# Performance work log

Hardware: AMD Instinct MI355X
Metric: run time of the kernel (lower is better)

## Reference

```python
import jax, jax.numpy as jnp
import numpy as np

NUM_EMBEDDINGS = 1024
EMBEDDING_DIM = 512
SAMPLE_TOKENS = 4
CODE_DIM = EMBEDDING_DIM // SAMPLE_TOKENS  # 128
COMMITMENT_COST = 0.25


def setup_inputs() -> dict:
    key = jax.random.key(0)
    k1, k2 = jax.random.split(key)
    inputs = jax.random.normal(k1, (16, 1024, EMBEDDING_DIM), dtype=jnp.float32)
    # nn.Embedding weight init: uniform(-1/K, 1/K)
    emb_weight = jax.random.uniform(
        k2, (NUM_EMBEDDINGS, CODE_DIM), dtype=jnp.float32,
        minval=-1.0 / NUM_EMBEDDINGS, maxval=1.0 / NUM_EMBEDDINGS)
    return {"inputs": inputs, "emb_weight": emb_weight}


def reference(inputs, emb_weight):
    input_shape = inputs.shape
    flat = inputs.reshape(-1, CODE_DIM)  # [N, d]
    distances = (jnp.sum(flat * flat, axis=1, keepdims=True)
                 + jnp.sum(emb_weight * emb_weight, axis=1)
                 - 2.0 * jnp.matmul(flat, emb_weight.T))  # [N, K]
    encoding_indices = jnp.argmin(distances, axis=1)  # [N]
    # gather codebook rows instead of one-hot matmul (same math)
    quantized = jnp.take(emb_weight, encoding_indices, axis=0).reshape(input_shape)

    e_latent_loss = jnp.mean((jax.lax.stop_gradient(quantized) - inputs) ** 2)
    q_latent_loss = jnp.mean((quantized - jax.lax.stop_gradient(inputs)) ** 2)
    loss = q_latent_loss + COMMITMENT_COST * e_latent_loss

    # straight-through estimator
    quantized_ste = inputs + jax.lax.stop_gradient(quantized - inputs)

    # avg_probs = mean of one-hot encodings = code-usage histogram / N
    n = flat.shape[0]
    counts = jnp.zeros((NUM_EMBEDDINGS,), dtype=jnp.float32).at[encoding_indices].add(1.0)
    avg_probs = counts / n
    perplexity = jnp.exp(-jnp.sum(avg_probs * jnp.log(avg_probs + 1e-10)))

    return (quantized_ste, loss, perplexity)
```

## Files before the change

### kernel.cpp

```cpp
#include <hip/hip_runtime.h>
#include <cmath>

#define DIM      128
#define NELEMS   8388608
#define BAND_INT 12288

typedef __attribute__((ext_vector_type(8))) short  short8;
typedef __attribute__((ext_vector_type(4))) float  f32x4;


__device__ inline unsigned short f2bf(float x) {
    unsigned u = __float_as_uint(x);
    unsigned r = u + 0x7FFFu + ((u >> 16) & 1u);
    return (unsigned short)(r >> 16);
}

__global__ __launch_bounds__(256) void vq_prep_kernel(
        const float* __restrict__ e, unsigned short* __restrict__ Ehi,
        float* __restrict__ Bsq, int* __restrict__ counts, double* __restrict__ sse) {
    const int tid = threadIdx.x;
    {
        const int t  = blockIdx.x * 256 + tid;
        const int c  = t >> 4;
        const int gs = t & 15;
        const int kt = gs >> 2, qd = gs & 3;
        const int d0 = gs * 8;
        const float4 v0 = *(const float4*)(e + c * DIM + d0);
        const float4 v1 = *(const float4*)(e + c * DIM + d0 + 4);
        float f[8] = {v0.x, v0.y, v0.z, v0.w, v1.x, v1.y, v1.z, v1.w};
        unsigned short h[8];
        #pragma unroll
        for (int j = 0; j < 8; ++j) h[j] = f2bf(f[j]);
        const int ct = c >> 4, n = c & 15;
        uint4 ph;
        ph.x = h[0] | (h[1] << 16); ph.y = h[2] | (h[3] << 16);
        ph.z = h[4] | (h[5] << 16); ph.w = h[6] | (h[7] << 16);
        *(uint4*)&Ehi[(((ct * 4 + kt) * 64 + qd * 16 + n) * 8)] = ph;
    }
    {
        const int lane = tid & 31;
        #pragma unroll
        for (int r2 = 0; r2 < 2; ++r2) {
            const int row = blockIdx.x * 16 + (tid >> 5) * 2 + r2;
            const float4 xv = *(const float4*)(e + (size_t)row * DIM + lane * 4);
            float s = xv.x * xv.x + xv.y * xv.y + xv.z * xv.z + xv.w * xv.w;
            #pragma unroll
            for (int off = 16; off > 0; off >>= 1) s += __shfl_xor(s, off);
            if (lane == 0) Bsq[row] = s;
        }
    }
    if (blockIdx.x == 0) {
        ((int4*)counts)[tid] = make_int4(0, 0, 0, 0);
        if (tid == 0) *sse = 0.0;
    }
}

#define LOADPAIR(BUF, P)                                                        \
    do {                                                                        \
        const unsigned short* _bp = Ehi + (size_t)(P) * 4096;                   \
        _Pragma("unroll")                                                       \
        for (int _c = 0; _c < 2; ++_c)                                          \
            _Pragma("unroll")                                                   \
            for (int _kt = 0; _kt < 4; ++_kt)                                   \
                BUF[_c][_kt] = *(const short8*)&_bp[((_c * 4 + _kt) * 64 + lane) * 8]; \
    } while (0)

#define COMPUTEPAIR(BUF, P)                                                     \
    do {                                                                        \
        _Pragma("unroll")                                                       \
        for (int _c = 0; _c < 2; ++_c) {                                        \
            const int _ct = 2 * (P) + _c;                                       \
            f32x4 _a0 = cinit, _a1 = cinit;                                     \
            _Pragma("unroll")                                                   \
            for (int _kt = 0; _kt < 4; ++_kt) {                                 \
                _a0 = __builtin_amdgcn_mfma_f32_16x16x32_bf16(Af[0][_kt], BUF[_c][_kt], _a0, 0, 0, 0); \
                _a1 = __builtin_amdgcn_mfma_f32_16x16x32_bf16(Af[1][_kt], BUF[_c][_kt], _a1, 0, 0, 0); \
            }                                                                   \
            _Pragma("unroll")                                                   \
            for (int _r = 0; _r < 4; ++_r) {                                    \
                const int _k0 = (__float_as_int(_a0[_r]) & (int)0xFFFFFFC0) | _ct; \
                const int _t0 = min(K1[_r], _k0);                               \
                K1[_r] = max(K1[_r], _k0);                                      \
                K2[_r] = max(K2[_r], _t0);                                      \
                const int _k1 = (__float_as_int(_a1[_r]) & (int)0xFFFFFFC0) | _ct; \
                const int _t1 = min(K1[4 + _r], _k1);                           \
                K1[4 + _r] = max(K1[4 + _r], _k1);                              \
                K2[4 + _r] = max(K2[4 + _r], _t1);                              \
            }                                                                   \
        }                                                                       \
    } while (0)

__global__ __launch_bounds__(256) void vq_main_kernel(
        const float* __restrict__ x, const float* __restrict__ emb,
        const unsigned short* __restrict__ Ehi, const float* __restrict__ Bsq,
        int* __restrict__ counts, double* __restrict__ sse,
        float* __restrict__ out) {
    __shared__ __align__(16) unsigned short Xs[8448];
    __shared__ float sAsq[64];
    __shared__ int   sidx[64];

    const int tid  = threadIdx.x;
    const int wave = tid >> 6;
    const int lane = tid & 63;
    const int n    = lane & 15;
    const int quad = lane >> 4;
    const int row0 = blockIdx.x * 64;

    {
        const int rl = tid >> 3, tq = tid & 7;
        const int dbase = tq * 16;
        const int rg_lo = rl >> 4, m = rl & 15;
        #pragma unroll
        for (int w = 0; w < 2; ++w) {
            const int r = 32 * w + rl;
            const float* xp = x + (size_t)(row0 + r) * DIM + dbase;
            float p[4];
            #pragma unroll
            for (int q = 0; q < 4; ++q) {
                const float4 v = *(const float4*)(xp + 4 * q);
                p[q] = v.x * v.x + v.y * v.y + v.z * v.z + v.w * v.w;
                const int dd = dbase + 4 * q;
                const int kt = dd >> 5, qd = (dd >> 3) & 3, j = dd & 7;
                unsigned short h0 = f2bf(v.x), h1 = f2bf(v.y), h2 = f2bf(v.z), h3 = f2bf(v.w);
                uint2 ph;
                ph.x = h0 | (h1 << 16); ph.y = h2 | (h3 << 16);
                const int rg = w * 2 + rg_lo;
                *(uint2*)&Xs[(((rg * 4 + kt) * 64 + qd * 16 + m) * 8) + j] = ph;
            }
            #pragma unroll
            for (int q = 0; q < 4; ++q) p[q] += __shfl_xor(p[q], 4);
            #pragma unroll
            for (int q = 0; q < 4; ++q) p[q] += __shfl_xor(p[q], 2);
            #pragma unroll
            for (int q = 0; q < 4; ++q) p[q] += __shfl_xor(p[q], 1);
            const float s = (p[0] + p[2]) + (p[1] + p[3]);
            if (tq == 0) sAsq[r] = s;
        }
    }
    __syncthreads();

    short8 Af[2][4];
    {
        const int h = wave & 1;
        #pragma unroll
        for (int rti = 0; rti < 2; ++rti)
            #pragma unroll
            for (int kt = 0; kt < 4; ++kt)
                Af[rti][kt] = *(const short8*)&Xs[((((h * 2 + rti) * 4 + kt) * 64 + lane) * 8)];
    }
    __syncthreads();

    int K1[8], K2[8];
    #pragma unroll
    for (int i = 0; i < 8; ++i) { K1[i] = (int)0x80000000; K2[i] = (int)0x80000000; }

    const f32x4 cinit = {1.0f, 1.0f, 1.0f, 1.0f};

    short8 BfA[2][4], BfB[2][4];
    const int pbase = (wave >> 1) * 16;
    LOADPAIR(BfA, pbase);
    for (int u = 0; u < 8; ++u) {
        const int pA = pbase + 2 * u, pB = pA + 1;
        LOADPAIR(BfB, pB);
        COMPUTEPAIR(BfA, pA);
        if (u < 7) LOADPAIR(BfA, pA + 2);
        COMPUTEPAIR(BfB, pB);
    }

    int2* sc = (int2*)Xs;
    #pragma unroll
    for (int r8 = 0; r8 < 8; ++r8) {
        const int lr = 32 * (wave & 1) + 16 * (r8 >> 2) + quad * 4 + (r8 & 3);
        sc[lr * 33 + (wave >> 1) * 16 + n] = make_int2(K1[r8], K2[r8]);
    }
    __syncthreads();

    if (tid < 64) {
        const int row  = tid;
        const int rowg = row0 + row;
        const int2* ent = (const int2*)sc + row * 33;
        int mx = (int)0x80000000;
        #pragma unroll
        for (int e2 = 0; e2 < 32; ++e2) mx = max(mx, ent[e2].x);
        const int thr = mx - BAND_INT;
        int ck[8];
        int nc = 0;
        #pragma unroll
        for (int e2 = 0; e2 < 32; ++e2) {
            const int2 kk = ent[e2];
            const int ne = e2 & 15;
            if (kk.x >= thr && nc < 8) ck[nc++] = ((kk.x & 63) << 4) | ne;
            if (kk.y >= thr && nc < 8) ck[nc++] = ((kk.y & 63) << 4) | ne;
        }
        float bd = INFINITY;
        int   bk = 0x7fffffff;
        const float4* xr = (const float4*)(x + (size_t)rowg * DIM);
        const float   aq = sAsq[row];
        for (int c = 0; c < nc; ++c) {
            const int k = ck[c];
            const float4* er = (const float4*)(emb + (size_t)k * DIM);
            float acc = 0.0f;
            #pragma unroll 4
            for (int dd = 0; dd < 32; ++dd) {
                const float4 xv = xr[dd];
                const float4 ev = er[dd];
                acc += xv.x * ev.x;
                acc += xv.y * ev.y;
                acc += xv.z * ev.z;
                acc += xv.w * ev.w;
            }
            const float t    = aq + Bsq[k];
            const float dist = t - 2.0f * acc;
            if (dist < bd || (dist == bd && k < bk)) { bd = dist; bk = k; }
        }
        sidx[row] = bk;
        atomicAdd(&counts[bk], 1);
        float ss = bd;
        #pragma unroll
        for (int off = 32; off > 0; off >>= 1) ss += __shfl_down(ss, off);
        if (tid == 0) atomicAdd(sse, (double)ss);
    }
    __syncthreads();

    #pragma unroll
    for (int i = tid; i < 2048; i += 256) {
        const int row = i >> 5, d4 = i & 31;
        const int k = sidx[row];
        const float4 xv = *((const float4*)(x + (size_t)(row0 + row) * DIM) + d4);
        const float4 qv = *((const float4*)emb + (size_t)k * 32 + d4);
        float4 ov;
        ov.x = xv.x + (qv.x - xv.x);
        ov.y = xv.y + (qv.y - xv.y);
        ov.z = xv.z + (qv.z - xv.z);
        ov.w = xv.w + (qv.w - xv.w);
        *((float4*)out + (size_t)(row0 + row) * 32 + d4) = ov;
    }
}

__global__ __launch_bounds__(1024) void vq_finalize_kernel(
        const int* __restrict__ counts, const double* __restrict__ sse,
        float* __restrict__ out_tail) {
    __shared__ double red[1024];
    const int t = threadIdx.x;
    const float p = (float)counts[t] * (1.0f / 65536.0f);
    red[t] = (double)p * log((double)p + 1e-10);
    __syncthreads();
    for (int s = 512; s > 0; s >>= 1) {
        if (t < s) red[t] += red[t + s];
        __syncthreads();
    }
    if (t == 0) {
        const float m = (float)(*sse * (1.0 / 8388608.0));
        out_tail[0] = m + 0.25f * m;
        out_tail[1] = (float)exp(-red[0]);
    }
}

extern "C" void kernel_launch(void* const* d_in, const int* in_sizes, int n_in,
                              void* d_out, int out_size, void* d_ws, size_t ws_size,
                              hipStream_t stream) {
    const float* x   = (const float*)d_in[0];
    const float* emb = (const float*)d_in[1];
    float* out = (float*)d_out;

    char*           ws     = (char*)d_ws;
    float*          Bsq    = (float*)(ws + 0);
    int*            counts = (int*)(ws + 4096);
    double*         sse    = (double*)(ws + 8192);
    unsigned short* Ehi    = (unsigned short*)(ws + 16384);

    vq_prep_kernel<<<64, 256, 0, stream>>>(emb, Ehi, Bsq, counts, sse);
    vq_main_kernel<<<1024, 256, 0, stream>>>(x, emb, Ehi, Bsq, counts, sse, out);
    vq_finalize_kernel<<<1, 1024, 0, stream>>>(counts, sse, out + NELEMS);
}
```

Before: 155.5 us.

## Fold finalize into main kernel via last-block counter; single-tile B pipeline

Removes the separate finalize launch: each main-kernel block bumps an atomic done counter, and the last block computes the perplexity and loss reductions. The codebook B-fragment pipeline also changes from double-buffered pairs of column tiles to single tiles, which halves the registers held for B. This trades one kernel launch and its dependency gap for a threadfence plus an atomic in every block, and adds a serial tail run by one block.

```diff
diff --git a/kernel.cpp b/kernel.cpp
--- a/kernel.cpp
+++ b/kernel.cpp
@@ -4,6 +4,7 @@
 #define DIM      128
 #define NELEMS   8388608
 #define BAND_INT 12288
+#define NBLOCKS  1024
 
 typedef __attribute__((ext_vector_type(8))) short  short8;
 typedef __attribute__((ext_vector_type(4))) float  f32x4;
@@ -17,7 +18,8 @@
 
 __global__ __launch_bounds__(256) void vq_prep_kernel(
         const float* __restrict__ e, unsigned short* __restrict__ Ehi,
-        float* __restrict__ Bsq, int* __restrict__ counts, double* __restrict__ sse) {
+        float* __restrict__ Bsq, int* __restrict__ counts, double* __restrict__ sse,
+        int* __restrict__ done) {
     const int tid = threadIdx.x;
     {
         const int t  = blockIdx.x * 256 + tid;
@@ -51,42 +53,37 @@
     }
     if (blockIdx.x == 0) {
         ((int4*)counts)[tid] = make_int4(0, 0, 0, 0);
-        if (tid == 0) *sse = 0.0;
-    }
-}
-
-#define LOADPAIR(BUF, P)                                                        \
+        if (tid == 0) { *sse = 0.0; *done = 0; }
+    }
+}
+
+#define LOADCT(BUF, C)                                                          \
     do {                                                                        \
-        const unsigned short* _bp = Ehi + (size_t)(P) * 4096;                   \
+        const unsigned short* _bp = Ehi + (size_t)(C) * 2048;                   \
         _Pragma("unroll")                                                       \
-        for (int _c = 0; _c < 2; ++_c)                                          \
-            _Pragma("unroll")                                                   \
-            for (int _kt = 0; _kt < 4; ++_kt)                                   \
-                BUF[_c][_kt] = *(const short8*)&_bp[((_c * 4 + _kt) * 64 + lane) * 8]; \
+        for (int _kt = 0; _kt < 4; ++_kt)                                       \
+            BUF[_kt] = *(const short8*)&_bp[(_kt * 64 + lane) * 8];             \
     } while (0)
 
-#define COMPUTEPAIR(BUF, P)                                                     \
+#define COMPUTECT(BUF, C)                                                       \
     do {                                                                        \
+        const int _ct = (C);                                                    \
+        f32x4 _a0 = cinit, _a1 = cinit;                                         \
         _Pragma("unroll")                                                       \
-        for (int _c = 0; _c < 2; ++_c) {                                        \
-            const int _ct = 2 * (P) + _c;                                       \
-            f32x4 _a0 = cinit, _a1 = cinit;                                     \
-            _Pragma("unroll")                                                   \
-            for (int _kt = 0; _kt < 4; ++_kt) {                                 \
-                _a0 = __builtin_amdgcn_mfma_f32_16x16x32_bf16(Af[0][_kt], BUF[_c][_kt], _a0, 0, 0, 0); \
-                _a1 = __builtin_amdgcn_mfma_f32_16x16x32_bf16(Af[1][_kt], BUF[_c][_kt], _a1, 0, 0, 0); \
-            }                                                                   \
-            _Pragma("unroll")                                                   \
-            for (int _r = 0; _r < 4; ++_r) {                                    \
-                const int _k0 = (__float_as_int(_a0[_r]) & (int)0xFFFFFFC0) | _ct; \
-                const int _t0 = min(K1[_r], _k0);                               \
-                K1[_r] = max(K1[_r], _k0);                                      \
-                K2[_r] = max(K2[_r], _t0);                                      \
-                const int _k1 = (__float_as_int(_a1[_r]) & (int)0xFFFFFFC0) | _ct; \
-                const int _t1 = min(K1[4 + _r], _k1);                           \
-                K1[4 + _r] = max(K1[4 + _r], _k1);                              \
-                K2[4 + _r] = max(K2[4 + _r], _t1);                              \
-            }                                                                   \
+        for (int _kt = 0; _kt < 4; ++_kt) {                                     \
+            _a0 = __builtin_amdgcn_mfma_f32_16x16x32_bf16(Af[0][_kt], BUF[_kt], _a0, 0, 0, 0); \
+            _a1 = __builtin_amdgcn_mfma_f32_16x16x32_bf16(Af[1][_kt], BUF[_kt], _a1, 0, 0, 0); \
+        }                                                                       \
+        _Pragma("unroll")                                                       \
+        for (int _r = 0; _r < 4; ++_r) {                                        \
+            const int _k0 = (__float_as_int(_a0[_r]) & (int)0xFFFFFFC0) | _ct;  \
+            const int _t0 = min(K1[_r], _k0);                                   \
+            K1[_r] = max(K1[_r], _k0);                                          \
+            K2[_r] = max(K2[_r], _t0);                                          \
+            const int _k1 = (__float_as_int(_a1[_r]) & (int)0xFFFFFFC0) | _ct;  \
+            const int _t1 = min(K1[4 + _r], _k1);                               \
+            K1[4 + _r] = max(K1[4 + _r], _k1);                                  \
+            K2[4 + _r] = max(K2[4 + _r], _t1);                                  \
         }                                                                       \
     } while (0)
 
@@ -94,10 +91,12 @@
         const float* __restrict__ x, const float* __restrict__ emb,
         const unsigned short* __restrict__ Ehi, const float* __restrict__ Bsq,
         int* __restrict__ counts, double* __restrict__ sse,
-        float* __restrict__ out) {
+        int* __restrict__ done, float* __restrict__ out) {
     __shared__ __align__(16) unsigned short Xs[8448];
-    __shared__ float sAsq[64];
-    __shared__ int   sidx[64];
+    __shared__ float  sAsq[64];
+    __shared__ int    sidx[64];
+    __shared__ int    sIsLast;
+    __shared__ double red[256];
 
     const int tid  = threadIdx.x;
     const int wave = tid >> 6;
@@ -156,15 +155,15 @@
 
     const f32x4 cinit = {1.0f, 1.0f, 1.0f, 1.0f};
 
-    short8 BfA[2][4], BfB[2][4];
-    const int pbase = (wave >> 1) * 16;
-    LOADPAIR(BfA, pbase);
-    for (int u = 0; u < 8; ++u) {
-        const int pA = pbase + 2 * u, pB = pA + 1;
-        LOADPAIR(BfB, pB);
-        COMPUTEPAIR(BfA, pA);
-        if (u < 7) LOADPAIR(BfA, pA + 2);
-        COMPUTEPAIR(BfB, pB);
+    short8 BfX[4], BfY[4];
+    const int c0 = (wave >> 1) * 32;
+    LOADCT(BfX, c0);
+    for (int u = 0; u < 16; ++u) {
+        const int cA = c0 + 2 * u, cB = cA + 1;
+        LOADCT(BfY, cB);
+        COMPUTECT(BfX, cA);
+        if (u < 15) LOADCT(BfX, cA + 2);
+        COMPUTECT(BfY, cB);
     }
 
     int2* sc = (int2*)Xs;
@@ -235,24 +234,29 @@
         ov.w = xv.w + (qv.w - xv.w);
         *((float4*)out + (size_t)(row0 + row) * 32 + d4) = ov;
     }
-}
-
-__global__ __launch_bounds__(1024) void vq_finalize_kernel(
-        const int* __restrict__ counts, const double* __restrict__ sse,
-        float* __restrict__ out_tail) {
-    __shared__ double red[1024];
-    const int t = threadIdx.x;
-    const float p = (float)counts[t] * (1.0f / 65536.0f);
-    red[t] = (double)p * log((double)p + 1e-10);
-    __syncthreads();
-    for (int s = 512; s > 0; s >>= 1) {
-        if (t < s) red[t] += red[t + s];
+
+    __threadfence();
+    if (tid == 0) sIsLast = (atomicAdd(done, 1) == NBLOCKS - 1);
+    __syncthreads();
+    if (sIsLast) {
+        __threadfence();
+        double s = 0.0;
+        #pragma unroll
+        for (int k = tid; k < 1024; k += 256) {
+            const float p = (float)counts[k] * (1.0f / 65536.0f);
+            s += (double)p * log((double)p + 1e-10);
+        }
+        red[tid] = s;
         __syncthreads();
-    }
-    if (t == 0) {
-        const float m = (float)(*sse * (1.0 / 8388608.0));
-        out_tail[0] = m + 0.25f * m;
-        out_tail[1] = (float)exp(-red[0]);
+        for (int st = 128; st > 0; st >>= 1) {
+            if (tid < st) red[tid] += red[tid + st];
+            __syncthreads();
+        }
+        if (tid == 0) {
+            const float m = (float)(*sse * (1.0 / 8388608.0));
+            out[NELEMS]     = m + 0.25f * m;
+            out[NELEMS + 1] = (float)exp(-red[0]);
+        }
     }
 }
 
@@ -267,9 +271,9 @@
     float*          Bsq    = (float*)(ws + 0);
     int*            counts = (int*)(ws + 4096);
     double*         sse    = (double*)(ws + 8192);
+    int*            done   = (int*)(ws + 12288);
     unsigned short* Ehi    = (unsigned short*)(ws + 16384);
 
-    vq_prep_kernel<<<64, 256, 0, stream>>>(emb, Ehi, Bsq, counts, sse);
-    vq_main_kernel<<<1024, 256, 0, stream>>>(x, emb, Ehi, Bsq, counts, sse, out);
-    vq_finalize_kernel<<<1, 1024, 0, stream>>>(counts, sse, out + NELEMS);
-}
+    vq_prep_kernel<<<64, 256, 0, stream>>>(emb, Ehi, Bsq, counts, sse, done);
+    vq_main_kernel<<<NBLOCKS, 256, 0, stream>>>(x, emb, Ehi, Bsq, counts, sse, done, out);
+}
```

After: 269.3 us. +73.2%, slower.
